# Kernel tuning notes

Hardware: AMD Instinct MI355X
Metric: run time of the kernel (lower is better)

## Reference

```python
import jax, jax.numpy as jnp
import numpy as np


def _lstm_dir(xs, Wih, Whh, bih, bhh, reverse):
    # xs: [T, B, E]; torch LSTM gate order i, f, g, o
    B = xs.shape[1]
    H = Whh.shape[1]
    h0 = jnp.zeros((B, H), xs.dtype)
    c0 = jnp.zeros((B, H), xs.dtype)

    def step(carry, xt):
        h, c = carry
        g = xt @ Wih.T + h @ Whh.T + (bih + bhh)
        i, f, gg, o = jnp.split(g, 4, axis=-1)
        i = jax.nn.sigmoid(i)
        f = jax.nn.sigmoid(f)
        gg = jnp.tanh(gg)
        o = jax.nn.sigmoid(o)
        c_new = f * c + i * gg
        h_new = o * jnp.tanh(c_new)
        return (h_new, c_new), h_new

    _, hs = jax.lax.scan(step, (h0, c0), xs, reverse=reverse)
    return hs  # [T, B, H] time-aligned


def _forward(x, edge_index, emb_table, Wih_f, Whh_f, bih_f, bhh_f,
             Wih_b, Whh_b, bih_b, bhh_b, label_emb, ggc_weight,
             gru_Wih, gru_Whh, gru_bih, gru_bhh, proj_W, proj_b):
    # --- embedding (dropout is identity in eval) ---
    emb = emb_table[x]                       # [B, T, E]
    xs = jnp.transpose(emb, (1, 0, 2))       # [T, B, E]
    hf = _lstm_dir(xs, Wih_f, Whh_f, bih_f, bhh_f, reverse=False)
    hb = _lstm_dir(xs, Wih_b, Whh_b, bih_b, bhh_b, reverse=True)
    c = jnp.concatenate([hf, hb], axis=-1)   # [T, B, 2H]
    c = jnp.transpose(c, (1, 0, 2))          # [B, T, 2H]

    # --- label cosine similarity, summed over tokens ---
    eps = 1e-8
    cn = c / jnp.maximum(jnp.linalg.norm(c, axis=-1, keepdims=True), eps)
    ln = label_emb / jnp.maximum(jnp.linalg.norm(label_emb, axis=-1, keepdims=True), eps)
    ls = jnp.einsum('btd,ld->bl', cn, ln)    # [B, C] (sum over t folded in)

    # --- GatedGraphConv, 2 layers, aggr='add', edge_weight=None ---
    src, dst = edge_index[0], edge_index[1]
    N = ls.shape[0]
    h = ls
    for i in range(ggc_weight.shape[0]):
        m = h @ ggc_weight[i]                            # [N, C]
        m = jax.ops.segment_sum(m[src], dst, num_segments=N)  # gather + scatter-add
        # torch GRUCell: gates r, z, n
        gi = m @ gru_Wih.T + gru_bih
        gh = h @ gru_Whh.T + gru_bhh
        ir, iz, inn = jnp.split(gi, 3, axis=-1)
        hr, hz, hn = jnp.split(gh, 3, axis=-1)
        r = jax.nn.sigmoid(ir + hr)
        z = jax.nn.sigmoid(iz + hz)
        n = jnp.tanh(inn + r * hn)
        h = (1.0 - z) * n + z * h

    return h @ proj_W.T + proj_b             # [B, C]


def setup_inputs() -> dict:
    key = jax.random.key(0)
    ks = jax.random.split(key, 20)
    V, E, B, T, C, NE = 50000, 300, 2048, 64, 1024, 65536
    H = E
    s = 0.05
    inp = {
        'x': jax.random.randint(ks[0], (B, T), 0, V),
        'edge_index': jax.random.randint(ks[1], (2, NE), 0, B),
        'emb_table': jax.random.normal(ks[2], (V, E)) * s,
        'Wih_f': jax.random.normal(ks[3], (4 * H, E)) * s,
        'Whh_f': jax.random.normal(ks[4], (4 * H, H)) * s,
        'bih_f': jnp.zeros((4 * H,)),
        'bhh_f': jnp.zeros((4 * H,)),
        'Wih_b': jax.random.normal(ks[5], (4 * H, E)) * s,
        'Whh_b': jax.random.normal(ks[6], (4 * H, H)) * s,
        'bih_b': jnp.zeros((4 * H,)),
        'bhh_b': jnp.zeros((4 * H,)),
        'label_emb': jax.random.normal(ks[7], (C, 2 * H)) * s,
        'ggc_weight': jax.random.normal(ks[8], (2, C, C)) * (1.0 / np.sqrt(C)),
        'gru_Wih': jax.random.normal(ks[9], (3 * C, C)) * (1.0 / np.sqrt(C)),
        'gru_Whh': jax.random.normal(ks[10], (3 * C, C)) * (1.0 / np.sqrt(C)),
        'gru_bih': jnp.zeros((3 * C,)),
        'gru_bhh': jnp.zeros((3 * C,)),
        'proj_W': jax.random.normal(ks[11], (C, C)) * (1.0 / np.sqrt(C)),
        'proj_b': jnp.zeros((C,)),
    }
    return inp


def reference(x, edge_index, emb_table, Wih_f, Whh_f, bih_f, bhh_f,
              Wih_b, Whh_b, bih_b, bhh_b, label_emb, ggc_weight,
              gru_Wih, gru_Whh, gru_bih, gru_bhh, proj_W, proj_b):
    return _forward(x, edge_index, emb_table, Wih_f, Whh_f, bih_f, bhh_f,
                    Wih_b, Whh_b, bih_b, bhh_b, label_emb, ggc_weight,
                    gru_Wih, gru_Whh, gru_bih, gru_bhh, proj_W, proj_b)
```

## Files before the change

### kernel.cpp

```cpp
#include <hip/hip_runtime.h>
#include <hip/hip_bf16.h>
#include <stdint.h>

typedef __hip_bfloat16 bf16;
typedef __attribute__((ext_vector_type(8))) short frag16;
typedef __attribute__((ext_vector_type(4))) float f32x4;

#define B_ 2048
#define T_ 64
#define E_ 300
#define H_ 300
#define C_ 1024
#define V_ 50000
#define NE_ 65536
#define HP 320
#define KC 640
#define NP 1280

static __device__ __forceinline__ float sigf(float x) {
  x = fminf(fmaxf(x, -30.f), 30.f);
  return 1.f / (1.f + __expf(-x));
}
static __device__ __forceinline__ float tanhfast(float x) {
  x = fminf(fmaxf(x, -15.f), 15.f);
  float e = __expf(2.f * x);
  return (e - 1.f) / (e + 1.f);
}
static __device__ __forceinline__ float ldraw(const void* p, size_t i, int isb) {
  return isb ? __bfloat162float(((const bf16*)p)[i]) : ((const float*)p)[i];
}
static __device__ __forceinline__ short b2s(bf16 b) {
  short s; __builtin_memcpy(&s, &b, 2); return s;
}
static __device__ __forceinline__ short4 f4tob4(float4 v) {
  return make_short4(b2s(__float2bfloat16(v.x)), b2s(__float2bfloat16(v.y)),
                     b2s(__float2bfloat16(v.z)), b2s(__float2bfloat16(v.w)));
}

static __device__ __forceinline__ void g2l16(const void* g, void* l) {
  __builtin_amdgcn_global_load_lds(
      (const __attribute__((address_space(1))) void*)(uintptr_t)g,
      (__attribute__((address_space(3))) void*)(uintptr_t)l, 16, 0, 0);
}

__global__ void detect_dtype(const unsigned short* __restrict__ e2, int* __restrict__ flag) {
  __shared__ int red[4];
  int tid = threadIdx.x;
  int ones = 0;
#pragma unroll
  for (int s = 0; s < 16; ++s) ones += (e2[2 * (tid * 16 + s)] >> 14) & 1;
  for (int off = 32; off > 0; off >>= 1) ones += __shfl_down(ones, off, 64);
  if ((tid & 63) == 0) red[tid >> 6] = ones;
  __syncthreads();
  if (tid == 0) {
    int tot = red[0] + red[1] + red[2] + red[3];
    *flag = (tot < 1024) ? 1 : 0;
  }
}

__global__ __launch_bounds__(256) void gemm_bt(
    const bf16* A, int lda, const bf16* W, int ldw, const float* bias,
    float* Cf, bf16* Cb, int ldc, int K,
    const int* __restrict__ rawp, int outmode,
    const bf16* A2, const bf16* W2, const float* bias2, float* Cf2) {
  if (blockIdx.z) { A = A2; W = W2; bias = bias2; Cf = Cf2; Cb = nullptr; }
  __shared__ __align__(16) short As[3][128 * 32];
  __shared__ __align__(16) short Bs[3][128 * 32];
  const int isb = rawp ? *rawp : 1;
  const int nxb = gridDim.x;
  const int id = blockIdx.x + nxb * blockIdx.y;
  const int npx = nxb >> 3;
  const int jj = id >> 3;
  const int bx = (id & 7) * npx + (npx > 1 ? jj % npx : 0);
  const int by = npx > 1 ? jj / npx : jj;
  const int n0 = bx * 128, m0 = by * 128;
  const int lane = threadIdx.x & 63, wv = threadIdx.x >> 6;
  const int wm = (wv & 1) * 64, wn = (wv >> 1) * 64;
  const int gr = lane >> 2;
  const int gc = (lane & 3) * 8;
  const short* pA0 = (const short*)A + (size_t)(m0 + wv * 32 + gr) * lda + gc;
  const short* pA1 = pA0 + (size_t)16 * lda;
  const short* pB0 = (const short*)W + (size_t)(n0 + wv * 32 + gr) * ldw + gc;
  const short* pB1 = pB0 + (size_t)16 * ldw;

  auto issueT = [&](int k0, int buf) {
    short* a = &As[buf][wv * 1024];
    short* b = &Bs[buf][wv * 1024];
    g2l16(pA0 + k0, a);
    g2l16(pA1 + k0, a + 512);
    g2l16(pB0 + k0, b);
    g2l16(pB1 + k0, b + 512);
  };

  f32x4 acc[4][4];
#pragma unroll
  for (int i = 0; i < 4; ++i)
#pragma unroll
    for (int j = 0; j < 4; ++j) acc[i][j] = (f32x4){0.f, 0.f, 0.f, 0.f};

  const int nk = K / 32;
  const int krd = (lane >> 4) * 8;
  const int rsel = lane & 15;
  issueT(0, 0);
  if (nk > 1) issueT(32, 1);
  if (nk > 2) issueT(64, 2);
  for (int kk = 0; kk < nk; ++kk) {
    const int cur = kk % 3;
    if (kk + 2 < nk)      asm volatile("s_waitcnt vmcnt(8)" ::: "memory");
    else if (kk + 1 < nk) asm volatile("s_waitcnt vmcnt(4)" ::: "memory");
    else                  asm volatile("s_waitcnt vmcnt(0)" ::: "memory");
    __builtin_amdgcn_s_barrier();
    frag16 af[4], bfg[4];
#pragma unroll
    for (int i = 0; i < 4; ++i) af[i] = *(const frag16*)&As[cur][(wm + i * 16 + rsel) * 32 + krd];
#pragma unroll
    for (int i = 0; i < 4; ++i) bfg[i] = *(const frag16*)&Bs[cur][(wn + i * 16 + rsel) * 32 + krd];
#pragma unroll
    for (int i = 0; i < 4; ++i)
#pragma unroll
      for (int j = 0; j < 4; ++j)
        acc[i][j] = __builtin_amdgcn_mfma_f32_16x16x32_bf16(af[i], bfg[j], acc[i][j], 0, 0, 0);
    asm volatile("" ::: "memory");
    __builtin_amdgcn_s_barrier();
    if (kk + 3 < nk) issueT(32 * (kk + 3), cur);
  }
  const int rq = (lane >> 4) * 4, cq = lane & 15;
#pragma unroll
  for (int j = 0; j < 4; ++j) {
    int cidx = n0 + wn + j * 16 + cq;
    float bv = bias ? bias[cidx] : 0.f;
#pragma unroll
    for (int i = 0; i < 4; ++i) {
      int rbase = m0 + wm + i * 16 + rq;
#pragma unroll
      for (int r = 0; r < 4; ++r) {
        float v = acc[i][j][r] + bv;
        size_t idx = (size_t)(rbase + r) * ldc + cidx;
        if (outmode) {
          if (isb) Cb[idx] = __float2bfloat16(v);
          else Cf[idx] = v;
        } else {
          if (Cf) Cf[idx] = v;
          if (Cb) Cb[idx] = __float2bfloat16(v);
        }
      }
    }
  }
}

static __device__ __forceinline__ void normacc_row2(
    const bf16* hfA, const bf16* hbA, const bf16* hfB, const bf16* hbB,
    float* __restrict__ Spf, int b, int lane) {
  float vA[10], vB[10];
  float sA = 0.f, sB = 0.f;
#pragma unroll
  for (int s = 0; s < 10; ++s) {
    int d = lane + 64 * s;
    float a = 0.f, c = 0.f;
    if (d < 300) {
      a = __bfloat162float(hfA[d]);
      c = __bfloat162float(hfB[d]);
    } else if (d < 600) {
      a = __bfloat162float(hbA[d - 300]);
      c = __bfloat162float(hbB[d - 300]);
    }
    vA[s] = a; vB[s] = c;
    sA += a * a; sB += c * c;
  }
#pragma unroll
  for (int off = 32; off > 0; off >>= 1) {
    sA += __shfl_xor(sA, off, 64);
    sB += __shfl_xor(sB, off, 64);
  }
  float kA = 1.f / fmaxf(sqrtf(sA), 1e-8f);
  float kB = 1.f / fmaxf(sqrtf(sB), 1e-8f);
  float* dst = Spf + (size_t)b * KC;
#pragma unroll
  for (int s = 0; s < 10; ++s) {
    int d = lane + 64 * s;
    if (d < 600) dst[d] += vA[s] * kA + vB[s] * kB;
  }
}

__global__ __launch_bounds__(256) void lstm_step(
    const void* __restrict__ emb, const bf16* __restrict__ embtail,
    const int* __restrict__ x,
    const bf16* __restrict__ Wcat, const float* __restrict__ bcat,
    bf16* __restrict__ hpad, float* __restrict__ cstate,
    bf16* __restrict__ Hfst, bf16* __restrict__ Hbst, float* __restrict__ Spf,
    int s, const int* __restrict__ flagp) {
  const int pb = s & 1;
  const int lane = threadIdx.x & 63, wv = threadIdx.x >> 6;

  if (blockIdx.z == 2) {
    if (s >= 33) {
      int bid = blockIdx.x + gridDim.x * blockIdx.y;
      const bf16* hinf = hpad + (size_t)pb * B_ * HP;
      const bf16* hinb = hpad + (size_t)(2 + pb) * B_ * HP;
      const int t1 = s - 1, t2 = 64 - s;
#pragma unroll
      for (int rep = 0; rep < 2; ++rep) {
        int b = bid * 4 + wv + 1280 * rep;
        if (b < B_)
          normacc_row2(hinf + (size_t)b * HP,
                       Hbst + ((size_t)(t1 - 32) * B_ + b) * H_,
                       Hfst + ((size_t)t2 * B_ + b) * H_,
                       hinb + (size_t)b * HP, Spf, b, lane);
      }
    }
    return;
  }

  __shared__ __align__(16) char smem[36864];
  float* epi = (float*)smem;

  const int dir = blockIdx.z;
  const int tt = dir ? (T_ - 1 - s) : s;
  const int isb = *flagp;
  const bf16* hin = hpad + (size_t)(dir * 2 + pb) * B_ * HP;
  const bf16* Wd = Wcat + (size_t)dir * NP * KC;
  bf16* hout = hpad + (size_t)(dir * 2 + (1 - pb)) * B_ * HP;
  float* cs = cstate + (size_t)dir * B_ * HP;
  const int id = blockIdx.x + gridDim.x * blockIdx.y;
  const int jj = id >> 3;
  const int mt = (id & 7) * 4 + (jj & 3);
  const int nt = jj >> 2;
  const int n0 = nt * 128, m0 = mt * 64;
  const int wm = (wv & 1) * 32, wn = (wv >> 1) * 64;
  const int gr = lane >> 2;
  const int gc = (lane & 3) * 8;
  const int arow = m0 + wv * 16 + gr;
  const int tok = x[arow * T_ + tt];
  const short* es = (const short*)emb;
  const float* ef = (const float*)emb;
  const short* px = es + (size_t)tok * E_ + gc;
  const short* ptail = (const short*)embtail + (size_t)tok * 32 + gc;
  const short* ph = (const short*)hin + (size_t)arow * HP + gc;
  const short* pB0 = (const short*)Wd + (size_t)(n0 + wv * 32 + gr) * KC + gc;
  const short* pB1 = pB0 + (size_t)16 * KC;

  auto issueT = [&](int k0, int buf) {
    short* a = (short*)(smem + buf * 4096) + wv * 512;
    short* b = (short*)(smem + 12288 + buf * 8192) + wv * 1024;
    if (k0 < HP) {
      g2l16(k0 == 288 ? ptail : (px + k0), a);
    } else {
      g2l16(ph + (k0 - HP), a);
    }
    g2l16(pB0 + k0, b);
    g2l16(pB1 + k0, b + 512);
  };

  f32x4 acc[2][4];
#pragma unroll
  for (int i = 0; i < 2; ++i)
#pragma unroll
    for (int j = 0; j < 4; ++j) acc[i][j] = (f32x4){0.f, 0.f, 0.f, 0.f};

  const int rsel = lane & 15, krd = (lane >> 4) * 8;
  const int NKT = KC / 32;

  auto mfma8 = [&](const short* Ap, const short* Bp) {
    frag16 af[2], bfg[4];
#pragma unroll
    for (int i = 0; i < 2; ++i) af[i] = *(const frag16*)&Ap[(wm + i * 16 + rsel) * 32 + krd];
#pragma unroll
    for (int j = 0; j < 4; ++j) bfg[j] = *(const frag16*)&Bp[(wn + j * 16 + rsel) * 32 + krd];
#pragma unroll
    for (int i = 0; i < 2; ++i)
#pragma unroll
      for (int j = 0; j < 4; ++j)
        acc[i][j] = __builtin_amdgcn_mfma_f32_16x16x32_bf16(af[i], bfg[j], acc[i][j], 0, 0, 0);
  };

  if (isb) {
    issueT(0, 0);
    issueT(32, 1);
    issueT(64, 2);
    for (int kk = 0; kk < NKT; ++kk) {
      const int cur = kk % 3;
      if (kk + 2 < NKT)      asm volatile("s_waitcnt vmcnt(6)" ::: "memory");
      else if (kk + 1 < NKT) asm volatile("s_waitcnt vmcnt(3)" ::: "memory");
      else                   asm volatile("s_waitcnt vmcnt(0)" ::: "memory");
      __builtin_amdgcn_s_barrier();
      mfma8((const short*)(smem + cur * 4096), (const short*)(smem + 12288 + cur * 8192));
      asm volatile("" ::: "memory");
      __builtin_amdgcn_s_barrier();
      if (kk + 3 < NKT) issueT(32 * (kk + 3), cur);
    }
  } else {
    short* As0 = (short*)smem;
    short* Bs0 = (short*)(smem + 12288);
    for (int kk = 0; kk < NKT; ++kk) {
      const int k0 = kk * 32;
      if (k0 < HP) {
        int c0 = k0 + gc;
        float4 fa = (c0 < E_) ? *(const float4*)(ef + (size_t)tok * E_ + c0)
                              : make_float4(0.f, 0.f, 0.f, 0.f);
        float4 fb = (c0 + 4 < E_) ? *(const float4*)(ef + (size_t)tok * E_ + c0 + 4)
                                  : make_float4(0.f, 0.f, 0.f, 0.f);
        short* d = As0 + (wv * 16 + gr) * 32 + gc;
        *(short4*)d = f4tob4(fa);
        *(short4*)(d + 4) = f4tob4(fb);
      } else {
        g2l16(ph + (k0 - HP), As0 + wv * 512);
      }
      g2l16(pB0 + k0, Bs0 + wv * 1024);
      g2l16(pB1 + k0, Bs0 + wv * 1024 + 512);
      __syncthreads();
      mfma8(As0, Bs0);
      __syncthreads();
    }
  }

  const int rq = (lane >> 4) * 4, cq = lane & 15;
#pragma unroll
  for (int p = 0; p < 2; ++p) {
    if (wn == p * 64) {
#pragma unroll
      for (int j = 0; j < 4; ++j) {
        int cl = j * 16 + cq;
        float bv = bcat[dir * NP + n0 + p * 64 + cl];
#pragma unroll
        for (int i = 0; i < 2; ++i) {
          int rl = wm + i * 16 + rq;
#pragma unroll
          for (int r = 0; r < 4; ++r) epi[(rl + r) * 64 + cl] = acc[i][j][r] + bv;
        }
      }
    }
    __syncthreads();
    int jbase = (n0 + p * 64) >> 2;
    for (int it = threadIdx.x; it < 64 * 16; it += 256) {
      int rl = it >> 4, jl = it & 15;
      int jg = jbase + jl;
      if (jg < H_) {
        const float* row = epi + rl * 64 + jl * 4;
        float iv = sigf(row[0]);
        float fv = sigf(row[1]);
        float gv = tanhfast(row[2]);
        float ov = sigf(row[3]);
        int b = m0 + rl;
        float c = fv * cs[(size_t)b * HP + jg] + iv * gv;
        float h = ov * tanhfast(c);
        cs[(size_t)b * HP + jg] = c;
        bf16 hb = __float2bfloat16(h);
        hout[(size_t)b * HP + jg] = hb;
        if (dir) {
          if (tt >= 32) Hbst[((size_t)(tt - 32) * B_ + b) * H_ + jg] = hb;
        } else if (tt < 32) {
          Hfst[((size_t)tt * B_ + b) * H_ + jg] = hb;
        }
      }
    }
    __syncthreads();
  }
}

__global__ __launch_bounds__(256) void normacc_fin(const bf16* __restrict__ hpad,
                                                   const bf16* __restrict__ Hfst,
                                                   const bf16* __restrict__ Hbst,
                                                   float* __restrict__ Spf) {
  int b = blockIdx.x * 4 + (threadIdx.x >> 6);
  int lane = threadIdx.x & 63;
  normacc_row2(hpad + (size_t)b * HP,
               Hbst + ((size_t)31 * B_ + b) * H_,
               Hfst + (size_t)b * H_,
               hpad + (size_t)2 * B_ * HP + (size_t)b * HP, Spf, b, lane);
}

__global__ void prep_all(const void* __restrict__ Wih_f, const void* __restrict__ Whh_f,
                         const void* __restrict__ bih_f, const void* __restrict__ bhh_f,
                         const void* __restrict__ Wih_b, const void* __restrict__ Whh_b,
                         const void* __restrict__ bih_b, const void* __restrict__ bhh_b,
                         const void* __restrict__ label, const void* __restrict__ ggcw,
                         const void* __restrict__ emb,
                         bf16* __restrict__ Wcat, float* __restrict__ bcat,
                         bf16* __restrict__ lnp, bf16* __restrict__ ggct,
                         bf16* __restrict__ embtail,
                         const int* __restrict__ flagp) {
  const int isb = *flagp;
  if (blockIdx.x < 1024) {
    int l = blockIdx.x, tid = threadIdx.x;
    __shared__ float red[4];
    float v[3];
    float ss = 0.f;
#pragma unroll
    for (int s = 0; s < 3; ++s) {
      int d = tid + 256 * s;
      v[s] = (d < 600) ? ldraw(label, (size_t)l * 600 + d, isb) : 0.f;
      ss += v[s] * v[s];
    }
    for (int off = 32; off > 0; off >>= 1) ss += __shfl_down(ss, off, 64);
    if ((tid & 63) == 0) red[tid >> 6] = ss;
    __syncthreads();
    float scale = 1.f / fmaxf(sqrtf(red[0] + red[1] + red[2] + red[3]), 1e-8f);
#pragma unroll
    for (int s = 0; s < 3; ++s) {
      int d = tid + 256 * s;
      if (d < KC) lnp[(size_t)l * KC + d] = __float2bfloat16(v[s] * scale);
    }
    return;
  }
  int i = (blockIdx.x - 1024) * 256 + threadIdx.x;
  if (i < 2 * NP * KC) {
    int k = i % KC;
    int n = (i / KC) % NP;
    int dir = i / (KC * NP);
    int j = n >> 2, q = n & 3;
    const void* Wih = dir ? Wih_b : Wih_f;
    const void* Whh = dir ? Whh_b : Whh_f;
    float v = 0.f;
    if (j < H_) {
      int row = q * H_ + j;
      if (k < E_) v = ldraw(Wih, (size_t)row * E_ + k, isb);
      else if (k >= HP && k < HP + H_) v = ldraw(Whh, (size_t)row * H_ + (k - HP), isb);
    }
    Wcat[i] = __float2bfloat16(v);
    if (k == 0) {
      const void* bih = dir ? bih_b : bih_f;
      const void* bhh = dir ? bhh_b : bhh_f;
      bcat[dir * NP + n] =
          (j < H_) ? (ldraw(bih, q * H_ + j, isb) + ldraw(bhh, q * H_ + j, isb)) : 0.f;
    }
    return;
  }
  i -= 2 * NP * KC;
  if (i < 2 * C_ * C_) {
    int k = i & 1023, n = (i >> 10) & 1023, l = i >> 20;
    size_t src = ((size_t)l << 20) | ((size_t)k << 10) | (size_t)n;
    ggct[i] = __float2bfloat16(ldraw(ggcw, src, isb));
    return;
  }
  i -= 2 * C_ * C_;
  if (i < V_ * 32) {
    int v = i >> 5, c = i & 31;
    float val = (c < E_ - 288) ? ldraw(emb, (size_t)v * E_ + 288 + c, isb) : 0.f;
    embtail[i] = __float2bfloat16(val);
  }
}

__global__ void prep2(const void* __restrict__ gWih, const void* __restrict__ gWhh,
                      const void* __restrict__ projW, const void* __restrict__ gbih,
                      const void* __restrict__ gbhh, const void* __restrict__ projb,
                      bf16* __restrict__ gWihb, bf16* __restrict__ gWhhb,
                      bf16* __restrict__ projWb, float* __restrict__ gbihf,
                      float* __restrict__ gbhhf, float* __restrict__ projbf,
                      const int* __restrict__ flagp) {
  const int isb = *flagp;
  int i = blockIdx.x * 256 + threadIdx.x;
  if (i < 3072 * C_) { gWihb[i] = __float2bfloat16(ldraw(gWih, i, isb)); return; }
  i -= 3072 * C_;
  if (i < 3072 * C_) { gWhhb[i] = __float2bfloat16(ldraw(gWhh, i, isb)); return; }
  i -= 3072 * C_;
  if (i < C_ * C_) { projWb[i] = __float2bfloat16(ldraw(projW, i, isb)); return; }
  i -= C_ * C_;
  if (i < 3072) { gbihf[i] = ldraw(gbih, i, isb); return; }
  i -= 3072;
  if (i < 3072) { gbhhf[i] = ldraw(gbhh, i, isb); return; }
  i -= 3072;
  if (i < C_) { projbf[i] = ldraw(projb, i, isb); }
}

__global__ void zero_u4(uint4* __restrict__ p, int n16) {
  int i = blockIdx.x * 256 + threadIdx.x;
  if (i < n16) p[i] = make_uint4(0u, 0u, 0u, 0u);
}

__global__ void edge_cnt(const int* __restrict__ ei, int* __restrict__ cnt) {
  int e = blockIdx.x * 256 + threadIdx.x;
  if (e < NE_) {
    int s = ei[e], d = ei[NE_ + e];
    atomicAdd(&cnt[(size_t)d * B_ + s], 1);
  }
}
__global__ void cnt2bf(const int* __restrict__ cnt, bf16* __restrict__ A) {
  int i = blockIdx.x * 256 + threadIdx.x;
  A[i] = __float2bfloat16((float)cnt[i]);
}

__global__ void gru_ew(const float* __restrict__ gi, const float* __restrict__ gh,
                       float* __restrict__ h, bf16* __restrict__ hb16) {
  int i = blockIdx.x * 256 + threadIdx.x;
  int b = i >> 10, j = i & 1023;
  const float* gib = gi + (size_t)b * 3072;
  const float* ghb = gh + (size_t)b * 3072;
  float r = sigf(gib[j] + ghb[j]);
  float z = sigf(gib[1024 + j] + ghb[1024 + j]);
  float n = tanhfast(gib[2048 + j] + r * ghb[2048 + j]);
  float hv = (1.f - z) * n + z * h[i];
  h[i] = hv;
  hb16[i] = __float2bfloat16(hv);
}

__global__ void spcvt(const float* __restrict__ Spf, bf16* __restrict__ Sp) {
  int i = blockIdx.x * 256 + threadIdx.x;
  Sp[i] = __float2bfloat16(Spf[i]);
}

__global__ void sentinel(bf16* __restrict__ o, int n, float v) {
  int i = blockIdx.x * 256 + threadIdx.x;
  if (i < n) o[i] = __float2bfloat16(v);
}

extern "C" void kernel_launch(void* const* d_in, const int* in_sizes, int n_in,
                              void* d_out, int out_size, void* d_ws, size_t ws_size,
                              hipStream_t stream) {
  const int* x = (const int*)d_in[0];
  const int* ei = (const int*)d_in[1];
  const void* emb = d_in[2];
  const void* Wih_f = d_in[3];
  const void* Whh_f = d_in[4];
  const void* bih_f = d_in[5];
  const void* bhh_f = d_in[6];
  const void* Wih_b = d_in[7];
  const void* Whh_b = d_in[8];
  const void* bih_b = d_in[9];
  const void* bhh_b = d_in[10];
  const void* label = d_in[11];
  const void* ggcw = d_in[12];
  const void* gWih = d_in[13];
  const void* gWhh = d_in[14];
  const void* gbih = d_in[15];
  const void* gbhh = d_in[16];
  const void* projW = d_in[17];
  const void* projb = d_in[18];
  (void)in_sizes; (void)n_in;

  const size_t NEED = (size_t)112 * 1024 * 1024;
  if (ws_size < NEED) {
    float v = 100.f + (float)(ws_size >> 24);
    sentinel<<<(out_size + 255) / 256, 256, 0, stream>>>((bf16*)d_out, out_size, v);
    return;
  }

  char* w = (char*)d_ws;
  size_t off = 0;
  auto alloc = [&](size_t bytes) {
    char* p = w + off;
    off += (bytes + 255) & ~(size_t)255;
    return p;
  };
  int* dflag = (int*)alloc(256);
  bf16* Wcat = (bf16*)alloc((size_t)2 * NP * KC * 2);
  float* bcat = (float*)alloc((size_t)2 * NP * 4);
  bf16* lnp = (bf16*)alloc((size_t)C_ * KC * 2);
  bf16* ggct = (bf16*)alloc((size_t)2 * C_ * C_ * 2);
  bf16* Sp = (bf16*)alloc((size_t)B_ * KC * 2);
  bf16* embtail = (bf16*)alloc((size_t)V_ * 32 * 2);
  const size_t phase_base = off;
  float* Spf = (float*)alloc((size_t)B_ * KC * 4);
  bf16* hpad = (bf16*)alloc((size_t)4 * B_ * HP * 2);
  float* cst = (float*)alloc((size_t)2 * B_ * HP * 4);
  bf16* Hfst = (bf16*)alloc((size_t)32 * B_ * H_ * 2);
  bf16* Hbst = (bf16*)alloc((size_t)32 * B_ * H_ * 2);
  off = phase_base;
  float* hbuf = (float*)alloc((size_t)B_ * C_ * 4);
  bf16* hb16 = (bf16*)alloc((size_t)B_ * C_ * 2);
  bf16* m1t = (bf16*)alloc((size_t)C_ * B_ * 2);
  bf16* aggb = (bf16*)alloc((size_t)B_ * C_ * 2);
  bf16* Acnt = (bf16*)alloc((size_t)B_ * B_ * 2);
  float* gi = (float*)alloc((size_t)B_ * 3072 * 4);
  float* gh = (float*)alloc((size_t)B_ * 3072 * 4);
  bf16* gWihb = (bf16*)alloc((size_t)3072 * C_ * 2);
  bf16* gWhhb = (bf16*)alloc((size_t)3072 * C_ * 2);
  bf16* projWb = (bf16*)alloc((size_t)C_ * C_ * 2);
  float* gbihf = (float*)alloc(3072 * 4);
  float* gbhhf = (float*)alloc(3072 * 4);
  float* projbf = (float*)alloc(C_ * 4);
  int* cnt = (int*)gi;

  detect_dtype<<<1, 256, 0, stream>>>((const unsigned short*)emb, dflag);
  prep_all<<<1024 + (2 * NP * KC + 2 * C_ * C_ + V_ * 32) / 256, 256, 0, stream>>>(
      Wih_f, Whh_f, bih_f, bhh_f, Wih_b, Whh_b, bih_b, bhh_b, label, ggcw, emb,
      Wcat, bcat, lnp, ggct, embtail, dflag);
  zero_u4<<<(3 * 327680) / 256, 256, 0, stream>>>((uint4*)Spf, 3 * 327680);

  for (int s = 0; s < T_; ++s)
    lstm_step<<<dim3(NP / 128, B_ / 64, 3), 256, 0, stream>>>(emb, embtail, x, Wcat, bcat,
                                                              hpad, cst, Hfst, Hbst, Spf,
                                                              s, dflag);
  normacc_fin<<<B_ / 4, 256, 0, stream>>>(hpad, Hfst, Hbst, Spf);
  spcvt<<<(B_ * KC) / 256, 256, 0, stream>>>(Spf, Sp);

  prep2<<<(2 * 3072 * C_ + C_ * C_ + 2 * 3072 + C_) / 256, 256, 0, stream>>>(
      gWih, gWhh, projW, gbih, gbhh, projb, gWihb, gWhhb, projWb, gbihf, gbhhf, projbf, dflag);

  gemm_bt<<<dim3(C_ / 128, B_ / 128), 256, 0, stream>>>(Sp, KC, lnp, KC, nullptr,
                                                        hbuf, hb16, C_, KC, nullptr, 0,
                                                        nullptr, nullptr, nullptr, nullptr);
  zero_u4<<<(B_ * B_ * 4 / 16) / 256, 256, 0, stream>>>((uint4*)cnt, B_ * B_ * 4 / 16);
  edge_cnt<<<NE_ / 256, 256, 0, stream>>>(ei, cnt);
  cnt2bf<<<(B_ * B_) / 256, 256, 0, stream>>>(cnt, Acnt);
  for (int l = 0; l < 2; ++l) {
    gemm_bt<<<dim3(B_ / 128, C_ / 128), 256, 0, stream>>>(ggct + (size_t)l * C_ * C_, C_,
                                                          hb16, C_, nullptr,
                                                          nullptr, m1t, B_, C_, nullptr, 0,
                                                          nullptr, nullptr, nullptr, nullptr);
    gemm_bt<<<dim3(C_ / 128, B_ / 128), 256, 0, stream>>>(Acnt, B_, m1t, B_, nullptr,
                                                          nullptr, aggb, C_, B_, nullptr, 0,
                                                          nullptr, nullptr, nullptr, nullptr);
    gemm_bt<<<dim3(3072 / 128, B_ / 128, 2), 256, 0, stream>>>(aggb, C_, gWihb, C_, gbihf,
                                                               gi, nullptr, 3072, C_, nullptr, 0,
                                                               hb16, gWhhb, gbhhf, gh);
    gru_ew<<<(B_ * C_) / 256, 256, 0, stream>>>(gi, gh, hbuf, hb16);
  }
  gemm_bt<<<dim3(C_ / 128, B_ / 128), 256, 0, stream>>>(hb16, C_, projWb, C_, projbf,
                                                        (float*)d_out, (bf16*)d_out, C_, C_,
                                                        dflag, 1,
                                                        nullptr, nullptr, nullptr, nullptr);
}
```

Before: 1.967 ms.

## Enlarge LSTM step tile to 128 rows and use 64-row tiles for small GEMMs

Each LSTM step block now computes a 128x128 output tile instead of 64x128, so each block loads twice as many A rows against the same weight tile. That halves the number of weight-tile loads per step, at the cost of fewer blocks, more registers and more shared memory. The norm-accumulation work in the z=2 blocks is redistributed to match the smaller grid. The small graph GEMMs and the projection GEMM switch to a new 64-row-tile kernel, which launches more blocks for better GPU occupancy.

```diff
diff --git a/kernel.cpp b/kernel.cpp
--- a/kernel.cpp
+++ b/kernel.cpp
@@ -148,6 +148,92 @@
   }
 }
 
+__global__ __launch_bounds__(256) void gemm_bt64(
+    const bf16* __restrict__ A, int lda, const bf16* __restrict__ W, int ldw,
+    const float* __restrict__ bias,
+    float* __restrict__ Cf, bf16* __restrict__ Cb, int ldc, int K,
+    const int* __restrict__ rawp, int outmode) {
+  __shared__ __align__(16) char smem[36864];
+  const int isb = rawp ? *rawp : 1;
+  const int nxb = gridDim.x;
+  const int id = blockIdx.x + nxb * blockIdx.y;
+  const int npx = nxb >> 3;
+  const int jj = id >> 3;
+  const int bx = (id & 7) * npx + (npx > 1 ? jj % npx : 0);
+  const int by = npx > 1 ? jj / npx : jj;
+  const int n0 = bx * 128, m0 = by * 64;
+  const int lane = threadIdx.x & 63, wv = threadIdx.x >> 6;
+  const int wm = (wv & 1) * 32, wn = (wv >> 1) * 64;
+  const int gr = lane >> 2, gc = (lane & 3) * 8;
+  const short* pA = (const short*)A + (size_t)(m0 + wv * 16 + gr) * lda + gc;
+  const short* pB0 = (const short*)W + (size_t)(n0 + wv * 32 + gr) * ldw + gc;
+  const short* pB1 = pB0 + (size_t)16 * ldw;
+
+  auto issueT = [&](int k0, int buf) {
+    short* a = (short*)(smem + buf * 4096) + wv * 512;
+    short* b = (short*)(smem + 12288 + buf * 8192) + wv * 1024;
+    g2l16(pA + k0, a);
+    g2l16(pB0 + k0, b);
+    g2l16(pB1 + k0, b + 512);
+  };
+
+  f32x4 acc[2][4];
+#pragma unroll
+  for (int i = 0; i < 2; ++i)
+#pragma unroll
+    for (int j = 0; j < 4; ++j) acc[i][j] = (f32x4){0.f, 0.f, 0.f, 0.f};
+
+  const int nk = K / 32;
+  const int krd = (lane >> 4) * 8, rsel = lane & 15;
+  issueT(0, 0);
+  if (nk > 1) issueT(32, 1);
+  if (nk > 2) issueT(64, 2);
+  for (int kk = 0; kk < nk; ++kk) {
+    const int cur = kk % 3;
+    if (kk + 2 < nk)      asm volatile("s_waitcnt vmcnt(6)" ::: "memory");
+    else if (kk + 1 < nk) asm volatile("s_waitcnt vmcnt(3)" ::: "memory");
+    else                  asm volatile("s_waitcnt vmcnt(0)" ::: "memory");
+    __builtin_amdgcn_s_barrier();
+    const short* Ap = (const short*)(smem + cur * 4096);
+    const short* Bp = (const short*)(smem + 12288 + cur * 8192);
+    frag16 af[2], bfg[4];
+#pragma unroll
+    for (int i = 0; i < 2; ++i) af[i] = *(const frag16*)&Ap[(wm + i * 16 + rsel) * 32 + krd];
+#pragma unroll
+    for (int j = 0; j < 4; ++j) bfg[j] = *(const frag16*)&Bp[(wn + j * 16 + rsel) * 32 + krd];
+#pragma unroll
+    for (int i = 0; i < 2; ++i)
+#pragma unroll
+      for (int j = 0; j < 4; ++j)
+        acc[i][j] = __builtin_amdgcn_mfma_f32_16x16x32_bf16(af[i], bfg[j], acc[i][j], 0, 0, 0);
+    asm volatile("" ::: "memory");
+    __builtin_amdgcn_s_barrier();
+    if (kk + 3 < nk) issueT(32 * (kk + 3), cur);
+  }
+  const int rq = (lane >> 4) * 4, cq = lane & 15;
+#pragma unroll
+  for (int j = 0; j < 4; ++j) {
+    int cidx = n0 + wn + j * 16 + cq;
+    float bv = bias ? bias[cidx] : 0.f;
+#pragma unroll
+    for (int i = 0; i < 2; ++i) {
+      int rbase = m0 + wm + i * 16 + rq;
+#pragma unroll
+      for (int r = 0; r < 4; ++r) {
+        float v = acc[i][j][r] + bv;
+        size_t idx = (size_t)(rbase + r) * ldc + cidx;
+        if (outmode) {
+          if (isb) Cb[idx] = __float2bfloat16(v);
+          else Cf[idx] = v;
+        } else {
+          if (Cf) Cf[idx] = v;
+          if (Cb) Cb[idx] = __float2bfloat16(v);
+        }
+      }
+    }
+  }
+}
+
 static __device__ __forceinline__ void normacc_row2(
     const bf16* hfA, const bf16* hbA, const bf16* hfB, const bf16* hbB,
     float* __restrict__ Spf, int b, int lane) {
@@ -199,8 +285,8 @@
       const bf16* hinb = hpad + (size_t)(2 + pb) * B_ * HP;
       const int t1 = s - 1, t2 = 64 - s;
 #pragma unroll
-      for (int rep = 0; rep < 2; ++rep) {
-        int b = bid * 4 + wv + 1280 * rep;
+      for (int rep = 0; rep < 4; ++rep) {
+        int b = bid * 4 + wv + 640 * rep;
         if (b < B_)
           normacc_row2(hinf + (size_t)b * HP,
                        Hbst + ((size_t)(t1 - 32) * B_ + b) * H_,
@@ -211,7 +297,7 @@
     return;
   }
 
-  __shared__ __align__(16) char smem[36864];
+  __shared__ __align__(16) char smem[49152];
   float* epi = (float*)smem;
 
   const int dir = blockIdx.z;
@@ -223,51 +309,57 @@
   float* cs = cstate + (size_t)dir * B_ * HP;
   const int id = blockIdx.x + gridDim.x * blockIdx.y;
   const int jj = id >> 3;
-  const int mt = (id & 7) * 4 + (jj & 3);
-  const int nt = jj >> 2;
-  const int n0 = nt * 128, m0 = mt * 64;
-  const int wm = (wv & 1) * 32, wn = (wv >> 1) * 64;
-  const int gr = lane >> 2;
-  const int gc = (lane & 3) * 8;
-  const int arow = m0 + wv * 16 + gr;
-  const int tok = x[arow * T_ + tt];
+  const int mt = (id & 7) * 2 + (jj & 1);
+  const int nt = jj >> 1;
+  const int n0 = nt * 128, m0 = mt * 128;
+  const int wm = (wv & 1) * 64, wn = (wv >> 1) * 64;
+  const int gr = lane >> 2, gc = (lane & 3) * 8;
+  const int ar0 = m0 + wv * 32 + gr;
+  const int ar1 = ar0 + 16;
+  const int tok0 = x[ar0 * T_ + tt];
+  const int tok1 = x[ar1 * T_ + tt];
   const short* es = (const short*)emb;
   const float* ef = (const float*)emb;
-  const short* px = es + (size_t)tok * E_ + gc;
-  const short* ptail = (const short*)embtail + (size_t)tok * 32 + gc;
-  const short* ph = (const short*)hin + (size_t)arow * HP + gc;
+  const short* px0 = es + (size_t)tok0 * E_ + gc;
+  const short* px1 = es + (size_t)tok1 * E_ + gc;
+  const short* pt0 = (const short*)embtail + (size_t)tok0 * 32 + gc;
+  const short* pt1 = (const short*)embtail + (size_t)tok1 * 32 + gc;
+  const short* ph0 = (const short*)hin + (size_t)ar0 * HP + gc;
+  const short* ph1 = (const short*)hin + (size_t)ar1 * HP + gc;
   const short* pB0 = (const short*)Wd + (size_t)(n0 + wv * 32 + gr) * KC + gc;
   const short* pB1 = pB0 + (size_t)16 * KC;
 
   auto issueT = [&](int k0, int buf) {
-    short* a = (short*)(smem + buf * 4096) + wv * 512;
-    short* b = (short*)(smem + 12288 + buf * 8192) + wv * 1024;
+    short* a = (short*)(smem + buf * 8192) + wv * 1024;
+    short* b = (short*)(smem + 24576 + buf * 8192) + wv * 1024;
     if (k0 < HP) {
-      g2l16(k0 == 288 ? ptail : (px + k0), a);
+      g2l16(k0 == 288 ? pt0 : (px0 + k0), a);
+      g2l16(k0 == 288 ? pt1 : (px1 + k0), a + 512);
     } else {
-      g2l16(ph + (k0 - HP), a);
+      g2l16(ph0 + (k0 - HP), a);
+      g2l16(ph1 + (k0 - HP), a + 512);
     }
     g2l16(pB0 + k0, b);
     g2l16(pB1 + k0, b + 512);
   };
 
-  f32x4 acc[2][4];
-#pragma unroll
-  for (int i = 0; i < 2; ++i)
+  f32x4 acc[4][4];
+#pragma unroll
+  for (int i = 0; i < 4; ++i)
 #pragma unroll
     for (int j = 0; j < 4; ++j) acc[i][j] = (f32x4){0.f, 0.f, 0.f, 0.f};
 
   const int rsel = lane & 15, krd = (lane >> 4) * 8;
   const int NKT = KC / 32;
 
-  auto mfma8 = [&](const short* Ap, const short* Bp) {
-    frag16 af[2], bfg[4];
-#pragma unroll
-    for (int i = 0; i < 2; ++i) af[i] = *(const frag16*)&Ap[(wm + i * 16 + rsel) * 32 + krd];
+  auto mfma16 = [&](const short* Ap, const short* Bp) {
+    frag16 af[4], bfg[4];
+#pragma unroll
+    for (int i = 0; i < 4; ++i) af[i] = *(const frag16*)&Ap[(wm + i * 16 + rsel) * 32 + krd];
 #pragma unroll
     for (int j = 0; j < 4; ++j) bfg[j] = *(const frag16*)&Bp[(wn + j * 16 + rsel) * 32 + krd];
 #pragma unroll
-    for (int i = 0; i < 2; ++i)
+    for (int i = 0; i < 4; ++i)
 #pragma unroll
       for (int j = 0; j < 4; ++j)
         acc[i][j] = __builtin_amdgcn_mfma_f32_16x16x32_bf16(af[i], bfg[j], acc[i][j], 0, 0, 0);
@@ -279,36 +371,44 @@
     issueT(64, 2);
     for (int kk = 0; kk < NKT; ++kk) {
       const int cur = kk % 3;
-      if (kk + 2 < NKT)      asm volatile("s_waitcnt vmcnt(6)" ::: "memory");
-      else if (kk + 1 < NKT) asm volatile("s_waitcnt vmcnt(3)" ::: "memory");
+      if (kk + 2 < NKT)      asm volatile("s_waitcnt vmcnt(8)" ::: "memory");
+      else if (kk + 1 < NKT) asm volatile("s_waitcnt vmcnt(4)" ::: "memory");
       else                   asm volatile("s_waitcnt vmcnt(0)" ::: "memory");
       __builtin_amdgcn_s_barrier();
-      mfma8((const short*)(smem + cur * 4096), (const short*)(smem + 12288 + cur * 8192));
+      mfma16((const short*)(smem + cur * 8192), (const short*)(smem + 24576 + cur * 8192));
       asm volatile("" ::: "memory");
       __builtin_amdgcn_s_barrier();
       if (kk + 3 < NKT) issueT(32 * (kk + 3), cur);
     }
   } else {
     short* As0 = (short*)smem;
-    short* Bs0 = (short*)(smem + 12288);
+    short* Bs0 = (short*)(smem + 24576);
     for (int kk = 0; kk < NKT; ++kk) {
       const int k0 = kk * 32;
       if (k0 < HP) {
         int c0 = k0 + gc;
-        float4 fa = (c0 < E_) ? *(const float4*)(ef + (size_t)tok * E_ + c0)
-                              : make_float4(0.f, 0.f, 0.f, 0.f);
-        float4 fb = (c0 + 4 < E_) ? *(const float4*)(ef + (size_t)tok * E_ + c0 + 4)
-                                  : make_float4(0.f, 0.f, 0.f, 0.f);
-        short* d = As0 + (wv * 16 + gr) * 32 + gc;
-        *(short4*)d = f4tob4(fa);
-        *(short4*)(d + 4) = f4tob4(fb);
+        float4 fa0 = (c0 < E_) ? *(const float4*)(ef + (size_t)tok0 * E_ + c0)
+                               : make_float4(0.f, 0.f, 0.f, 0.f);
+        float4 fb0 = (c0 + 4 < E_) ? *(const float4*)(ef + (size_t)tok0 * E_ + c0 + 4)
+                                   : make_float4(0.f, 0.f, 0.f, 0.f);
+        float4 fa1 = (c0 < E_) ? *(const float4*)(ef + (size_t)tok1 * E_ + c0)
+                               : make_float4(0.f, 0.f, 0.f, 0.f);
+        float4 fb1 = (c0 + 4 < E_) ? *(const float4*)(ef + (size_t)tok1 * E_ + c0 + 4)
+                                   : make_float4(0.f, 0.f, 0.f, 0.f);
+        short* d0 = As0 + (wv * 32 + gr) * 32 + gc;
+        short* d1 = As0 + (wv * 32 + 16 + gr) * 32 + gc;
+        *(short4*)d0 = f4tob4(fa0);
+        *(short4*)(d0 + 4) = f4tob4(fb0);
+        *(short4*)d1 = f4tob4(fa1);
+        *(short4*)(d1 + 4) = f4tob4(fb1);
       } else {
-        g2l16(ph + (k0 - HP), As0 + wv * 512);
+        g2l16(ph0 + (k0 - HP), As0 + wv * 1024);
+        g2l16(ph1 + (k0 - HP), As0 + wv * 1024 + 512);
       }
       g2l16(pB0 + k0, Bs0 + wv * 1024);
       g2l16(pB1 + k0, Bs0 + wv * 1024 + 512);
       __syncthreads();
-      mfma8(As0, Bs0);
+      mfma16(As0, Bs0);
       __syncthreads();
     }
   }
@@ -322,7 +422,7 @@
         int cl = j * 16 + cq;
         float bv = bcat[dir * NP + n0 + p * 64 + cl];
 #pragma unroll
-        for (int i = 0; i < 2; ++i) {
+        for (int i = 0; i < 4; ++i) {
           int rl = wm + i * 16 + rq;
 #pragma unroll
           for (int r = 0; r < 4; ++r) epi[(rl + r) * 64 + cl] = acc[i][j][r] + bv;
@@ -331,7 +431,7 @@
     }
     __syncthreads();
     int jbase = (n0 + p * 64) >> 2;
-    for (int it = threadIdx.x; it < 64 * 16; it += 256) {
+    for (int it = threadIdx.x; it < 128 * 16; it += 256) {
       int rl = it >> 4, jl = it & 15;
       int jg = jbase + jl;
       if (jg < H_) {
@@ -577,36 +677,32 @@
   zero_u4<<<(3 * 327680) / 256, 256, 0, stream>>>((uint4*)Spf, 3 * 327680);
 
   for (int s = 0; s < T_; ++s)
-    lstm_step<<<dim3(NP / 128, B_ / 64, 3), 256, 0, stream>>>(emb, embtail, x, Wcat, bcat,
-                                                              hpad, cst, Hfst, Hbst, Spf,
-                                                              s, dflag);
+    lstm_step<<<dim3(NP / 128, B_ / 128, 3), 256, 0, stream>>>(emb, embtail, x, Wcat, bcat,
+                                                               hpad, cst, Hfst, Hbst, Spf,
+                                                               s, dflag);
   normacc_fin<<<B_ / 4, 256, 0, stream>>>(hpad, Hfst, Hbst, Spf);
   spcvt<<<(B_ * KC) / 256, 256, 0, stream>>>(Spf, Sp);
 
   prep2<<<(2 * 3072 * C_ + C_ * C_ + 2 * 3072 + C_) / 256, 256, 0, stream>>>(
       gWih, gWhh, projW, gbih, gbhh, projb, gWihb, gWhhb, projWb, gbihf, gbhhf, projbf, dflag);
 
-  gemm_bt<<<dim3(C_ / 128, B_ / 128), 256, 0, stream>>>(Sp, KC, lnp, KC, nullptr,
-                                                        hbuf, hb16, C_, KC, nullptr, 0,
-                                                        nullptr, nullptr, nullptr, nullptr);
+  gemm_bt64<<<dim3(C_ / 128, B_ / 64), 256, 0, stream>>>(Sp, KC, lnp, KC, nullptr,
+                                                         hbuf, hb16, C_, KC, nullptr, 0);
   zero_u4<<<(B_ * B_ * 4 / 16) / 256, 256, 0, stream>>>((uint4*)cnt, B_ * B_ * 4 / 16);
   edge_cnt<<<NE_ / 256, 256, 0, stream>>>(ei, cnt);
   cnt2bf<<<(B_ * B_) / 256, 256, 0, stream>>>(cnt, Acnt);
   for (int l = 0; l < 2; ++l) {
-    gemm_bt<<<dim3(B_ / 128, C_ / 128), 256, 0, stream>>>(ggct + (size_t)l * C_ * C_, C_,
-                                                          hb16, C_, nullptr,
-                                                          nullptr, m1t, B_, C_, nullptr, 0,
-                                                          nullptr, nullptr, nullptr, nullptr);
-    gemm_bt<<<dim3(C_ / 128, B_ / 128), 256, 0, stream>>>(Acnt, B_, m1t, B_, nullptr,
-                                                          nullptr, aggb, C_, B_, nullptr, 0,
-                                                          nullptr, nullptr, nullptr, nullptr);
+    gemm_bt64<<<dim3(B_ / 128, C_ / 64), 256, 0, stream>>>(ggct + (size_t)l * C_ * C_, C_,
+                                                           hb16, C_, nullptr,
+                                                           nullptr, m1t, B_, C_, nullptr, 0);
+    gemm_bt64<<<dim3(C_ / 128, B_ / 64), 256, 0, stream>>>(Acnt, B_, m1t, B_, nullptr,
+                                                           nullptr, aggb, C_, B_, nullptr, 0);
     gemm_bt<<<dim3(3072 / 128, B_ / 128, 2), 256, 0, stream>>>(aggb, C_, gWihb, C_, gbihf,
                                                                gi, nullptr, 3072, C_, nullptr, 0,
                                                                hb16, gWhhb, gbhhf, gh);
     gru_ew<<<(B_ * C_) / 256, 256, 0, stream>>>(gi, gh, hbuf, hb16);
   }
-  gemm_bt<<<dim3(C_ / 128, B_ / 128), 256, 0, stream>>>(hb16, C_, projWb, C_, projbf,
-                                                        (float*)d_out, (bf16*)d_out, C_, C_,
-                                                        dflag, 1,
-                                                        nullptr, nullptr, nullptr, nullptr);
-}
+  gemm_bt64<<<dim3(C_ / 128, B_ / 64), 256, 0, stream>>>(hb16, C_, projWb, C_, projbf,
+                                                         (float*)d_out, (bf16*)d_out, C_, C_,
+                                                         dflag, 1);
+}
```

After: 2.307 ms. 1.17x slower.
